# Kernel optimization log

Hardware: AMD Instinct MI355X
Metric: run time of the kernel (lower is better)

Reference implementation:

```python
import jax, jax.numpy as jnp
import numpy as np

B, L, D = 4096, 50, 128          # users, neighbors/user, embed_dim
N_U, N_I, N_R, N_T = 10000, 100000, 6, 1000
EPS = 1e-5                       # BatchNorm eps (eval mode, running stats)


def setup_inputs() -> dict:
    key = jax.random.key(0)
    ks = iter(jax.random.split(key, 80))
    nk = lambda: next(ks)

    def lin(din, dout):
        s = 1.0 / np.sqrt(din)
        w = jax.random.uniform(nk(), (din, dout), minval=-s, maxval=s, dtype=jnp.float32)
        b = jax.random.uniform(nk(), (dout,), minval=-s, maxval=s, dtype=jnp.float32)
        return w, b

    inp = {}
    # embedding tables (u2e/i2e/r2e/t2e)
    inp['u2e'] = 0.1 * jax.random.normal(nk(), (N_U, D), jnp.float32)
    inp['i2e'] = 0.1 * jax.random.normal(nk(), (N_I, D), jnp.float32)
    inp['r2e'] = 0.1 * jax.random.normal(nk(), (N_R, D), jnp.float32)
    inp['t2e'] = 0.1 * jax.random.normal(nk(), (N_T, D), jnp.float32)
    # neighbor transform MLP
    inp['ne_w'], inp['ne_b'] = lin(3 * D, D)
    inp['ne1_w'], inp['ne1_b'] = lin(D, D)
    # attention MLP (NewAttention: concat(neigh, user) -> D -> D -> 1, softmax over neighbors)
    inp['att1_w'], inp['att1_b'] = lin(2 * D, D)
    inp['att2_w'], inp['att2_b'] = lin(D, D)
    inp['att3_w'], inp['att3_b'] = lin(D, 1)
    # head
    inp['lin_w'], inp['lin_b'] = lin(2 * D, D)
    inp['w1_w'], inp['w1_b'] = lin(D, D // 4)
    inp['bn1_g'] = jnp.ones((D // 4,), jnp.float32)
    inp['bn1_b'] = jnp.zeros((D // 4,), jnp.float32)
    inp['bn1_m'] = 0.1 * jax.random.normal(nk(), (D // 4,), jnp.float32)
    inp['bn1_v'] = jax.random.uniform(nk(), (D // 4,), minval=0.5, maxval=1.5, dtype=jnp.float32)
    inp['w2_w'], inp['w2_b'] = lin(D // 4, D // 8)
    inp['bn2_g'] = jnp.ones((D // 8,), jnp.float32)
    inp['bn2_b'] = jnp.zeros((D // 8,), jnp.float32)
    inp['bn2_m'] = 0.1 * jax.random.normal(nk(), (D // 8,), jnp.float32)
    inp['bn2_v'] = jax.random.uniform(nk(), (D // 8,), minval=0.5, maxval=1.5, dtype=jnp.float32)
    inp['w3_w'], inp['w3_b'] = lin(D // 8, 1)
    # index inputs (padded-fixed neighbor lists)
    inp['user_idx'] = jax.random.randint(nk(), (B,), 0, N_U)
    inp['item_idx'] = jax.random.randint(nk(), (B, L), 0, N_I)
    inp['rat_idx'] = jax.random.randint(nk(), (B, L), 0, N_R)
    inp['time_idx'] = jax.random.randint(nk(), (B, L), 0, N_T)
    return inp


def reference(u2e, i2e, r2e, t2e, ne_w, ne_b, ne1_w, ne1_b,
              att1_w, att1_b, att2_w, att2_b, att3_w, att3_b,
              lin_w, lin_b, w1_w, w1_b, bn1_g, bn1_b, bn1_m, bn1_v,
              w2_w, w2_b, bn2_g, bn2_b, bn2_m, bn2_v, w3_w, w3_b,
              user_idx, item_idx, rat_idx, time_idx):
    u = u2e[user_idx]                                                   # [B, D]
    neigh = jnp.concatenate([i2e[item_idx], r2e[rat_idx], t2e[time_idx]], axis=-1)  # [B, L, 3D]
    x = jax.nn.relu(neigh @ ne_w + ne_b)                                # [B, L, D]
    x = jax.nn.relu(x @ ne1_w + ne1_b)                                  # [B, L, D]
    # attention over neighbors, conditioned on the user embedding
    a = jnp.concatenate([x, jnp.broadcast_to(u[:, None, :], x.shape)], axis=-1)  # [B, L, 2D]
    a = jax.nn.relu(a @ att1_w + att1_b)
    a = jax.nn.relu(a @ att2_w + att2_b)
    att = jax.nn.softmax((a @ att3_w + att3_b)[..., 0], axis=-1)        # [B, L]
    pooled = jnp.einsum('bl,bld->bd', att, x)                           # torch.mm(x.t(), att).t()
    comb = jax.nn.relu(jnp.concatenate([u, pooled], axis=-1) @ lin_w + lin_b)  # [B, D]
    h = comb @ w1_w + w1_b
    h = jax.nn.relu((h - bn1_m) * jax.lax.rsqrt(bn1_v + EPS) * bn1_g + bn1_b)
    h = h @ w2_w + w2_b
    h = jax.nn.relu((h - bn2_m) * jax.lax.rsqrt(bn2_v + EPS) * bn2_g + bn2_b)
    return (h @ w3_w + w3_b)[:, 0]                                      # [B]
```

## Files before the change

kernel.cpp:

```cpp
#include <hip/hip_runtime.h>
#include <hip/hip_bf16.h>

typedef __bf16 bf16x8 __attribute__((ext_vector_type(8)));
typedef float  f32x4  __attribute__((ext_vector_type(4)));

#define W_OFF 0
#define A_OFF 16384
#define X_OFF 29696
#define SMALL 43008
#define SMEM_TOTAL 47104
#define WCHUNK 16384
#define WHALF  8192

#define WS_WPREP 0
#define WS_PI    262144
#define WS_PT    (WS_PI + 25600000)
#define WS_PR    (WS_PT + 512000)
#define WS_PU    (WS_PR + 3072)
#define WS_PU2   (WS_PU + 5120000)

__global__ void prep_weights_kernel(const float* __restrict__ ne_w,
                                    const float* __restrict__ ne1_w,
                                    const float* __restrict__ att1_w,
                                    const float* __restrict__ att2_w,
                                    const float* __restrict__ lin_w,
                                    __hip_bfloat16* __restrict__ wout) {
  __shared__ float tile[64][65];
  const int bx = blockIdx.x;
  const int c = bx >> 2, kt = (bx >> 1) & 1, ntile = bx & 1;
  const float* src; int koff;
  if      (c < 3)  { src = ne_w;   koff = c * 128; }
  else if (c == 3) { src = ne1_w;  koff = 0; }
  else if (c == 4) { src = att1_w; koff = 0; }
  else if (c == 5) { src = att2_w; koff = 0; }
  else if (c == 6) { src = att1_w; koff = 128; }
  else             { src = lin_w;  koff = 0; }
  const int tx = threadIdx.x, ty = threadIdx.y;
#pragma unroll
  for (int r = 0; r < 16; ++r) {
    int k = kt * 64 + r * 4 + ty, n = ntile * 64 + tx;
    tile[r * 4 + ty][tx] = src[(koff + k) * 128 + n];
  }
  __syncthreads();
#pragma unroll
  for (int r = 0; r < 16; ++r) {
    int n = ntile * 64 + r * 4 + ty, k = kt * 64 + tx;
    int h = k >> 6, k64 = k & 63;
    int off = c * WCHUNK + h * WHALF + n * 64 + ((((k64 >> 3) ^ (n & 7))) << 3) + (k64 & 7);
    wout[off] = __float2bfloat16(tile[tx][r * 4 + ty]);
  }
}

__device__ __forceinline__ unsigned short bf_bits(float x) {
  return __builtin_bit_cast(unsigned short, __float2bfloat16(x));
}

__device__ __forceinline__ void mfma_half(const __hip_bfloat16* sIn,
                                          const __hip_bfloat16* sWh,
                                          f32x4 acc[4], int h, int m16, int nh, int lane) {
  const int mr = lane & 15;
  const int kq = lane >> 4;
  const int arow = (m16 * 16 + mr) * 128;
#pragma unroll
  for (int ks = 0; ks < 2; ++ks) {
    const int kb16 = h * 8 + ks * 4 + kq;
    bf16x8 a = *(const bf16x8*)(sIn + arow + ((kb16 ^ mr) << 3));
    const int swzb = (((ks * 4 + kq) ^ (mr & 7)) << 3);
#pragma unroll
    for (int nt = 0; nt < 4; ++nt) {
      const int n = nh * 64 + nt * 16 + mr;
      bf16x8 b = *(const bf16x8*)(sWh + n * 64 + swzb);
      acc[nt] = __builtin_amdgcn_mfma_f32_16x16x32_bf16(a, b, acc[nt], 0, 0, 0);
    }
  }
}

__device__ __forceinline__ void epilogue(f32x4 acc[4], const float* __restrict__ bias,
                                         const float* addvec, __hip_bfloat16* sOut,
                                         int m16, int nh, int lane) {
  const int mr = lane & 15;
  const int rb = m16 * 16 + ((lane >> 4) << 2);
#pragma unroll
  for (int nt = 0; nt < 4; ++nt) {
    const int col = nh * 64 + nt * 16 + mr;
    float bv = bias[col];
    if (addvec) bv += addvec[col];
    const int cblk = col >> 3, clo = col & 7;
#pragma unroll
    for (int r = 0; r < 4; ++r) {
      const int row = rb + r;
      if (row < 50) {
        float v = fmaxf(acc[nt][r] + bv, 0.0f);
        sOut[row * 128 + ((cblk ^ (row & 15)) << 3) + clo] = __float2bfloat16(v);
      }
    }
  }
}

__global__ __launch_bounds__(512) void pgemm_kernel(
    const float* __restrict__ i2e, const float* __restrict__ r2e,
    const float* __restrict__ t2e, const float* __restrict__ u2e,
    const float* __restrict__ ne_b, const __hip_bfloat16* __restrict__ wprep,
    __hip_bfloat16* __restrict__ Pi, float* __restrict__ Pt, float* __restrict__ Pr,
    float* __restrict__ Pu, float* __restrict__ Pu2) {
  __shared__ __align__(16) __hip_bfloat16 sW[WCHUNK];
  __shared__ __align__(16) __hip_bfloat16 sA[64 * 128];
  const int tid = threadIdx.x, lane = tid & 63, wid = tid >> 6;
  const int m16 = wid & 3, nh = wid >> 2;
  const int bx = blockIdx.x;
  const float* src; const __hip_bfloat16* W; float* dst = nullptr;
  const float* addb = nullptr; bool bf_out = false;
  long rows0; int nrows;
  if (bx < 1563)      { src = i2e; W = wprep + 0 * WCHUNK; bf_out = true; rows0 = (long)bx * 64;          nrows = 100000; }
  else if (bx < 1579) { src = t2e; W = wprep + 2 * WCHUNK; dst = Pt;  rows0 = (long)(bx - 1563) * 64; nrows = 1000; }
  else if (bx < 1580) { src = r2e; W = wprep + 1 * WCHUNK; dst = Pr;  rows0 = 0;                      nrows = 6; addb = ne_b; }
  else if (bx < 1737) { src = u2e; W = wprep + 6 * WCHUNK; dst = Pu;  rows0 = (long)(bx - 1580) * 64; nrows = 10000; }
  else                { src = u2e; W = wprep + 7 * WCHUNK; dst = Pu2; rows0 = (long)(bx - 1737) * 64; nrows = 10000; }

#pragma unroll
  for (int i = 0; i < 4; ++i) {
    int g = tid + i * 512;
    __builtin_amdgcn_global_load_lds(
        (__attribute__((address_space(1))) void*)(void*)(W + g * 8),
        (__attribute__((address_space(3))) void*)(void*)(sW + g * 8), 16, 0, 0);
  }
  const float4* s4 = (const float4*)src;
#pragma unroll
  for (int i = 0; i < 2; ++i) {
    int g = tid + i * 512;
    int row = g >> 4, kb = g & 15;
    float4 v0 = {0.f, 0.f, 0.f, 0.f}, v1 = {0.f, 0.f, 0.f, 0.f};
    if (rows0 + row < nrows) {
      long base = (rows0 + row) * 32 + kb * 2;
      v0 = s4[base]; v1 = s4[base + 1];
    }
    uint4 pk;
    pk.x = ((unsigned)bf_bits(v0.y) << 16) | bf_bits(v0.x);
    pk.y = ((unsigned)bf_bits(v0.w) << 16) | bf_bits(v0.z);
    pk.z = ((unsigned)bf_bits(v1.y) << 16) | bf_bits(v1.x);
    pk.w = ((unsigned)bf_bits(v1.w) << 16) | bf_bits(v1.z);
    *(uint4*)(sA + row * 128 + ((kb ^ (row & 15)) << 3)) = pk;
  }
  __syncthreads();

  f32x4 acc[4];
#pragma unroll
  for (int j = 0; j < 4; ++j) acc[j] = (f32x4){0.f, 0.f, 0.f, 0.f};
  mfma_half(sA, sW, acc, 0, m16, nh, lane);
  mfma_half(sA, sW + WHALF, acc, 1, m16, nh, lane);

  const int mr = lane & 15;
  const int rb = m16 * 16 + ((lane >> 4) << 2);
#pragma unroll
  for (int nt = 0; nt < 4; ++nt) {
    const int col = nh * 64 + nt * 16 + mr;
    const float bv = addb ? addb[col] : 0.f;
#pragma unroll
    for (int r = 0; r < 4; ++r) {
      const int row = rb + r;
      if (rows0 + row < nrows) {
        if (bf_out) Pi[(rows0 + row) * 128 + col] = __float2bfloat16(acc[nt][r]);
        else        dst[(rows0 + row) * 128 + col] = acc[nt][r] + bv;
      }
    }
  }
}

__global__ __launch_bounds__(512, 6) void graphdec_main(
    const __hip_bfloat16* __restrict__ Pi, const float* __restrict__ Pt,
    const float* __restrict__ Pr, const float* __restrict__ Pu,
    const float* __restrict__ Pu2,
    const float* __restrict__ ne1_b, const float* __restrict__ att1_b,
    const float* __restrict__ att2_b, const float* __restrict__ att3_w,
    const float* __restrict__ lin_w, const float* __restrict__ lin_b,
    const float* __restrict__ w1_w, const float* __restrict__ w1_b,
    const float* __restrict__ bn1_g, const float* __restrict__ bn1_b,
    const float* __restrict__ bn1_m, const float* __restrict__ bn1_v,
    const float* __restrict__ w2_w, const float* __restrict__ w2_b,
    const float* __restrict__ bn2_g, const float* __restrict__ bn2_b,
    const float* __restrict__ bn2_m, const float* __restrict__ bn2_v,
    const float* __restrict__ w3_w, const float* __restrict__ w3_b,
    const int* __restrict__ user_idx, const int* __restrict__ item_idx,
    const int* __restrict__ rat_idx, const int* __restrict__ time_idx,
    const __hip_bfloat16* __restrict__ wprep, float* __restrict__ out) {
  __shared__ __align__(16) unsigned char smem[SMEM_TOTAL];
  __hip_bfloat16* sW = (__hip_bfloat16*)(smem + W_OFF);
  __hip_bfloat16* sA = (__hip_bfloat16*)(smem + A_OFF);
  __hip_bfloat16* sX = (__hip_bfloat16*)(smem + X_OFF);
  int*   sIdx   = (int*)  (smem + SMALL);
  float* sUatt  = (float*)(smem + SMALL + 768);
  float* sUlin  = (float*)(smem + SMALL + 1280);
  float* sLP0   = (float*)(smem + SMALL + 1792);
  float* sLP1   = (float*)(smem + SMALL + 2048);
  float* sAtt   = (float*)(smem + SMALL + 2304);
  float* sPooled= (float*)(smem + SMALL + 2560);
  float* sComb  = (float*)(smem + SMALL + 3072);
  float* sH1    = (float*)(smem + SMALL + 3584);
  float* sPool4 = (float*)(smem + W_OFF);
  float* sCombP = (float*)(smem + W_OFF + 2048);

  const int tid  = threadIdx.x;
  const int lane = tid & 63;
  const int wid  = tid >> 6;
  const int m16  = wid & 3;
  const int nh   = wid >> 2;
  const int b    = blockIdx.x;

  float att3r[4];
#pragma unroll
  for (int nt = 0; nt < 4; ++nt) att3r[nt] = att3_w[nh * 64 + nt * 16 + (lane & 15)];

  if (tid < 192) {
    int c = tid >> 6, l = tid & 63;
    int v = 0;
    if (l < 50) {
      const int* p = (c == 0) ? item_idx : (c == 1) ? rat_idx : time_idx;
      v = p[b * 50 + l];
    }
    sIdx[tid] = v;
  }
  const int uid = user_idx[b];
  if (tid >= 256 && tid < 384)      sUatt[tid - 256] = Pu [(long)uid * 128 + (tid - 256)];
  else if (tid >= 384)              sUlin[tid - 384] = Pu2[(long)uid * 128 + (tid - 384)];
  __syncthreads();

  auto stage16 = [&](const __hip_bfloat16* __restrict__ src) {
#pragma unroll
    for (int i = 0; i < 2; ++i) {
      int g = tid + i * 512;
      __builtin_amdgcn_global_load_lds(
          (__attribute__((address_space(1))) void*)(void*)(src + g * 8),
          (__attribute__((address_space(3))) void*)(void*)(sW + g * 8), 16, 0, 0);
    }
  };

  f32x4 acc[4];
  const f32x4 zf = {0.f, 0.f, 0.f, 0.f};
  auto zacc = [&]() {
#pragma unroll
    for (int j = 0; j < 4; ++j) acc[j] = zf;
  };

  stage16(wprep + 3 * WCHUNK);
#pragma unroll
  for (int i = 0; i < 2; ++i) {
    int g = tid + i * 512;
    if (g < 832) {
      int row = g >> 4, kb = g & 15;
      uint4 pk = {0u, 0u, 0u, 0u};
      if (row < 50) {
        const bf16x8 pv = *(const bf16x8*)(Pi + (long)sIdx[row] * 128 + kb * 8);
        const float4* pr4 = (const float4*)(Pr + (long)sIdx[64 + row] * 128) + kb * 2;
        const float4* pt4 = (const float4*)(Pt + (long)sIdx[128 + row] * 128) + kb * 2;
        float4 r0 = pr4[0], r1 = pr4[1];
        float4 t0 = pt4[0], t1 = pt4[1];
        float s0 = fmaxf((float)pv[0] + r0.x + t0.x, 0.f);
        float s1 = fmaxf((float)pv[1] + r0.y + t0.y, 0.f);
        float s2 = fmaxf((float)pv[2] + r0.z + t0.z, 0.f);
        float s3 = fmaxf((float)pv[3] + r0.w + t0.w, 0.f);
        float s4 = fmaxf((float)pv[4] + r1.x + t1.x, 0.f);
        float s5 = fmaxf((float)pv[5] + r1.y + t1.y, 0.f);
        float s6 = fmaxf((float)pv[6] + r1.z + t1.z, 0.f);
        float s7 = fmaxf((float)pv[7] + r1.w + t1.w, 0.f);
        pk.x = ((unsigned)bf_bits(s1) << 16) | bf_bits(s0);
        pk.y = ((unsigned)bf_bits(s3) << 16) | bf_bits(s2);
        pk.z = ((unsigned)bf_bits(s5) << 16) | bf_bits(s4);
        pk.w = ((unsigned)bf_bits(s7) << 16) | bf_bits(s6);
      }
      *(uint4*)(sA + row * 128 + ((kb ^ (row & 15)) << 3)) = pk;
    }
  }
  __syncthreads();

  zacc();
  mfma_half(sA, sW, acc, 0, m16, nh, lane);
  __syncthreads();
  stage16(wprep + 3 * WCHUNK + WHALF);
  __syncthreads();
  mfma_half(sA, sW, acc, 1, m16, nh, lane);
  __syncthreads();
  stage16(wprep + 4 * WCHUNK);
  epilogue(acc, ne1_b, nullptr, sX, m16, nh, lane);
  __syncthreads();

  zacc();
  mfma_half(sX, sW, acc, 0, m16, nh, lane);
  __syncthreads();
  stage16(wprep + 4 * WCHUNK + WHALF);
  __syncthreads();
  mfma_half(sX, sW, acc, 1, m16, nh, lane);
  __syncthreads();
  stage16(wprep + 5 * WCHUNK);
  epilogue(acc, att1_b, sUatt, sA, m16, nh, lane);
  __syncthreads();

  zacc();
  mfma_half(sA, sW, acc, 0, m16, nh, lane);
  __syncthreads();
  stage16(wprep + 5 * WCHUNK + WHALF);
  __syncthreads();
  mfma_half(sA, sW, acc, 1, m16, nh, lane);
  {
    float lp[4] = {0.f, 0.f, 0.f, 0.f};
#pragma unroll
    for (int nt = 0; nt < 4; ++nt) {
      const int col = nh * 64 + nt * 16 + (lane & 15);
      const float b2 = att2_b[col];
#pragma unroll
      for (int r = 0; r < 4; ++r)
        lp[r] += fmaxf(acc[nt][r] + b2, 0.f) * att3r[nt];
    }
#pragma unroll
    for (int off = 1; off < 16; off <<= 1) {
#pragma unroll
      for (int r = 0; r < 4; ++r) lp[r] += __shfl_xor(lp[r], off);
    }
    if ((lane & 15) == 0) {
      const int rowb = m16 * 16 + ((lane >> 4) << 2);
      float* dst = nh ? sLP1 : sLP0;
#pragma unroll
      for (int r = 0; r < 4; ++r) dst[rowb + r] = lp[r];
    }
  }
  __syncthreads();

  if (wid == 0) {
    float v = (lane < 50) ? (sLP0[lane] + sLP1[lane]) : -3.4e38f;
    float m = v;
    for (int off = 32; off > 0; off >>= 1) m = fmaxf(m, __shfl_xor(m, off));
    float e = (lane < 50) ? __expf(v - m) : 0.f;
    float s = e;
    for (int off = 32; off > 0; off >>= 1) s += __shfl_xor(s, off);
    sAtt[lane] = e / s;
  }
  __syncthreads();

  {
    int q = tid >> 7, d = tid & 127;
    const int cblk = d >> 3, clo = d & 7;
    float s = 0.f;
    for (int l = q; l < 50; l += 4)
      s += sAtt[l] * (float)sX[l * 128 + ((cblk ^ (l & 15)) << 3) + clo];
    sPool4[q * 128 + d] = s;
  }
  __syncthreads();
  if (tid < 128)
    sPooled[tid] = sPool4[tid] + sPool4[128 + tid] + sPool4[256 + tid] + sPool4[384 + tid];
  __syncthreads();

  {
    int q = tid >> 7, d = tid & 127;
    float s = 0.f;
    for (int j = q * 32; j < q * 32 + 32; ++j) s += sPooled[j] * lin_w[(128 + j) * 128 + d];
    sCombP[q * 128 + d] = s;
  }
  __syncthreads();
  if (tid < 128)
    sComb[tid] = fmaxf(sCombP[tid] + sCombP[128 + tid] + sCombP[256 + tid] + sCombP[384 + tid]
                       + sUlin[tid] + lin_b[tid], 0.f);
  __syncthreads();

  if (wid == 0) {
    if (lane < 32) {
      float s = w1_b[lane];
      for (int k = 0; k < 128; ++k) s += sComb[k] * w1_w[k * 32 + lane];
      s = (s - bn1_m[lane]) * rsqrtf(bn1_v[lane] + 1e-5f) * bn1_g[lane] + bn1_b[lane];
      sH1[lane] = fmaxf(s, 0.f);
    }
    if (lane < 16) {
      float s = w2_b[lane];
      for (int k = 0; k < 32; ++k) s += sH1[k] * w2_w[k * 16 + lane];
      s = (s - bn2_m[lane]) * rsqrtf(bn2_v[lane] + 1e-5f) * bn2_g[lane] + bn2_b[lane];
      float p = fmaxf(s, 0.f) * w3_w[lane];
      p += __shfl_xor(p, 1); p += __shfl_xor(p, 2);
      p += __shfl_xor(p, 4); p += __shfl_xor(p, 8);
      if (lane == 0) out[b] = p + w3_b[0];
    }
  }
}

extern "C" void kernel_launch(void* const* d_in, const int* in_sizes, int n_in,
                              void* d_out, int out_size, void* d_ws, size_t ws_size,
                              hipStream_t stream) {
  const float* u2e    = (const float*)d_in[0];
  const float* i2e    = (const float*)d_in[1];
  const float* r2e    = (const float*)d_in[2];
  const float* t2e    = (const float*)d_in[3];
  const float* ne_w   = (const float*)d_in[4];
  const float* ne_b   = (const float*)d_in[5];
  const float* ne1_w  = (const float*)d_in[6];
  const float* ne1_b  = (const float*)d_in[7];
  const float* att1_w = (const float*)d_in[8];
  const float* att1_b = (const float*)d_in[9];
  const float* att2_w = (const float*)d_in[10];
  const float* att2_b = (const float*)d_in[11];
  const float* att3_w = (const float*)d_in[12];
  const float* att3_b = (const float*)d_in[13];
  const float* lin_w  = (const float*)d_in[14];
  const float* lin_b  = (const float*)d_in[15];
  const float* w1_w   = (const float*)d_in[16];
  const float* w1_b   = (const float*)d_in[17];
  const float* bn1_g  = (const float*)d_in[18];
  const float* bn1_b  = (const float*)d_in[19];
  const float* bn1_m  = (const float*)d_in[20];
  const float* bn1_v  = (const float*)d_in[21];
  const float* w2_w   = (const float*)d_in[22];
  const float* w2_b   = (const float*)d_in[23];
  const float* bn2_g  = (const float*)d_in[24];
  const float* bn2_b  = (const float*)d_in[25];
  const float* bn2_m  = (const float*)d_in[26];
  const float* bn2_v  = (const float*)d_in[27];
  const float* w3_w   = (const float*)d_in[28];
  const float* w3_b   = (const float*)d_in[29];
  const int* user_idx = (const int*)d_in[30];
  const int* item_idx = (const int*)d_in[31];
  const int* rat_idx  = (const int*)d_in[32];
  const int* time_idx = (const int*)d_in[33];
  (void)att3_b;

  char* ws = (char*)d_ws;
  __hip_bfloat16* wprep = (__hip_bfloat16*)(ws + WS_WPREP);
  __hip_bfloat16* Pi = (__hip_bfloat16*)(ws + WS_PI);
  float* Pt  = (float*)(ws + WS_PT);
  float* Pr  = (float*)(ws + WS_PR);
  float* Pu  = (float*)(ws + WS_PU);
  float* Pu2 = (float*)(ws + WS_PU2);
  float* out = (float*)d_out;

  prep_weights_kernel<<<32, dim3(64, 4), 0, stream>>>(ne_w, ne1_w, att1_w, att2_w,
                                                      lin_w, wprep);
  pgemm_kernel<<<1894, 512, 0, stream>>>(i2e, r2e, t2e, u2e, ne_b, wprep,
                                         Pi, Pt, Pr, Pu, Pu2);
  graphdec_main<<<4096, 512, 0, stream>>>(
      Pi, Pt, Pr, Pu, Pu2, ne1_b, att1_b, att2_b, att3_w,
      lin_w, lin_b, w1_w, w1_b, bn1_g, bn1_b, bn1_m, bn1_v, w2_w, w2_b,
      bn2_g, bn2_b, bn2_m, bn2_v, w3_w, w3_b,
      user_idx, item_idx, rat_idx, time_idx, wprep, out);
}
```

Measured before the change: 242.3 us.

## Process two users per block to share staged weight tiles

Each graphdec_main block now handles two users instead of one. Four waves serve each user, and each wave computes all 128 output columns (8 MFMA tiles) rather than splitting N across waves. Every weight chunk staged into LDS is therefore reused across two users, which halves the weight staging traffic and the number of blocks. The cost is more LDS per block (about 77KB), twice the accumulator registers, and a lowered occupancy hint (4 instead of 6), which may reduce latency hiding for the gathers.

```diff
diff --git a/kernel.cpp b/kernel.cpp
--- a/kernel.cpp
+++ b/kernel.cpp
@@ -6,9 +6,9 @@
 
 #define W_OFF 0
 #define A_OFF 16384
-#define X_OFF 29696
-#define SMALL 43008
-#define SMEM_TOTAL 47104
+#define X_OFF 43008
+#define SMALL 69632
+#define SMEM_TOTAL 77824
 #define WCHUNK 16384
 #define WHALF  8192
 
@@ -55,6 +55,48 @@
   return __builtin_bit_cast(unsigned short, __float2bfloat16(x));
 }
 
+__device__ __forceinline__ void mfma_half8(const __hip_bfloat16* sIn,
+                                           const __hip_bfloat16* sWh,
+                                           f32x4 acc[8], int h, int m16, int lane) {
+  const int mr = lane & 15;
+  const int kq = lane >> 4;
+  const int arow = (m16 * 16 + mr) * 128;
+#pragma unroll
+  for (int ks = 0; ks < 2; ++ks) {
+    const int kb16 = h * 8 + ks * 4 + kq;
+    bf16x8 a = *(const bf16x8*)(sIn + arow + ((kb16 ^ mr) << 3));
+    const int swzb = (((ks * 4 + kq) ^ (mr & 7)) << 3);
+#pragma unroll
+    for (int nt = 0; nt < 8; ++nt) {
+      const int n = nt * 16 + mr;
+      bf16x8 b = *(const bf16x8*)(sWh + n * 64 + swzb);
+      acc[nt] = __builtin_amdgcn_mfma_f32_16x16x32_bf16(a, b, acc[nt], 0, 0, 0);
+    }
+  }
+}
+
+__device__ __forceinline__ void epilogue8(f32x4 acc[8], const float* __restrict__ bias,
+                                          const float* addvec, __hip_bfloat16* sOut,
+                                          int m16, int lane) {
+  const int mr = lane & 15;
+  const int rb = m16 * 16 + ((lane >> 4) << 2);
+#pragma unroll
+  for (int nt = 0; nt < 8; ++nt) {
+    const int col = nt * 16 + mr;
+    float bv = bias[col];
+    if (addvec) bv += addvec[col];
+    const int cblk = col >> 3, clo = col & 7;
+#pragma unroll
+    for (int r = 0; r < 4; ++r) {
+      const int row = rb + r;
+      if (row < 50) {
+        float v = fmaxf(acc[nt][r] + bv, 0.0f);
+        sOut[row * 128 + ((cblk ^ (row & 15)) << 3) + clo] = __float2bfloat16(v);
+      }
+    }
+  }
+}
+
 __device__ __forceinline__ void mfma_half(const __hip_bfloat16* sIn,
                                           const __hip_bfloat16* sWh,
                                           f32x4 acc[4], int h, int m16, int nh, int lane) {
@@ -71,28 +113,6 @@
       const int n = nh * 64 + nt * 16 + mr;
       bf16x8 b = *(const bf16x8*)(sWh + n * 64 + swzb);
       acc[nt] = __builtin_amdgcn_mfma_f32_16x16x32_bf16(a, b, acc[nt], 0, 0, 0);
-    }
-  }
-}
-
-__device__ __forceinline__ void epilogue(f32x4 acc[4], const float* __restrict__ bias,
-                                         const float* addvec, __hip_bfloat16* sOut,
-                                         int m16, int nh, int lane) {
-  const int mr = lane & 15;
-  const int rb = m16 * 16 + ((lane >> 4) << 2);
-#pragma unroll
-  for (int nt = 0; nt < 4; ++nt) {
-    const int col = nh * 64 + nt * 16 + mr;
-    float bv = bias[col];
-    if (addvec) bv += addvec[col];
-    const int cblk = col >> 3, clo = col & 7;
-#pragma unroll
-    for (int r = 0; r < 4; ++r) {
-      const int row = rb + r;
-      if (row < 50) {
-        float v = fmaxf(acc[nt][r] + bv, 0.0f);
-        sOut[row * 128 + ((cblk ^ (row & 15)) << 3) + clo] = __float2bfloat16(v);
-      }
     }
   }
 }
@@ -166,7 +186,7 @@
   }
 }
 
-__global__ __launch_bounds__(512, 6) void graphdec_main(
+__global__ __launch_bounds__(512, 4) void graphdec_main(
     const __hip_bfloat16* __restrict__ Pi, const float* __restrict__ Pt,
     const float* __restrict__ Pr, const float* __restrict__ Pu,
     const float* __restrict__ Pu2,
@@ -185,43 +205,54 @@
     const __hip_bfloat16* __restrict__ wprep, float* __restrict__ out) {
   __shared__ __align__(16) unsigned char smem[SMEM_TOTAL];
   __hip_bfloat16* sW = (__hip_bfloat16*)(smem + W_OFF);
-  __hip_bfloat16* sA = (__hip_bfloat16*)(smem + A_OFF);
-  __hip_bfloat16* sX = (__hip_bfloat16*)(smem + X_OFF);
-  int*   sIdx   = (int*)  (smem + SMALL);
-  float* sUatt  = (float*)(smem + SMALL + 768);
-  float* sUlin  = (float*)(smem + SMALL + 1280);
-  float* sLP0   = (float*)(smem + SMALL + 1792);
-  float* sLP1   = (float*)(smem + SMALL + 2048);
-  float* sAtt   = (float*)(smem + SMALL + 2304);
-  float* sPooled= (float*)(smem + SMALL + 2560);
-  float* sComb  = (float*)(smem + SMALL + 3072);
-  float* sH1    = (float*)(smem + SMALL + 3584);
-  float* sPool4 = (float*)(smem + W_OFF);
-  float* sCombP = (float*)(smem + W_OFF + 2048);
 
   const int tid  = threadIdx.x;
   const int lane = tid & 63;
   const int wid  = tid >> 6;
+  const int uw   = wid >> 2;
   const int m16  = wid & 3;
-  const int nh   = wid >> 2;
-  const int b    = blockIdx.x;
-
-  float att3r[4];
-#pragma unroll
-  for (int nt = 0; nt < 4; ++nt) att3r[nt] = att3_w[nh * 64 + nt * 16 + (lane & 15)];
-
-  if (tid < 192) {
-    int c = tid >> 6, l = tid & 63;
+  const int ut   = tid >> 8;
+  const int t256 = tid & 255;
+  const long b   = blockIdx.x;
+
+  __hip_bfloat16* sAw = (__hip_bfloat16*)(smem + A_OFF + uw * 13312);
+  __hip_bfloat16* sXw = (__hip_bfloat16*)(smem + X_OFF + uw * 13312);
+  __hip_bfloat16* sAt = (__hip_bfloat16*)(smem + A_OFF + ut * 13312);
+  __hip_bfloat16* sXt = (__hip_bfloat16*)(smem + X_OFF + ut * 13312);
+  unsigned char* sSmW = smem + SMALL + uw * 4096;
+  unsigned char* sSmT = smem + SMALL + ut * 4096;
+  int*   sIdxT   = (int*)  (sSmT);
+  float* sUattW  = (float*)(sSmW + 768);
+  float* sUlinT  = (float*)(sSmT + 1280);
+  float* sLPW    = (float*)(sSmW + 1792);
+  float* sLPU    = (float*)(sSmW + 1792);
+  float* sAttT   = (float*)(sSmT + 2048);
+  float* sPooledT= (float*)(sSmT + 2304);
+  float* sCombT  = (float*)(sSmT + 2816);
+  float* sCombW  = (float*)(sSmW + 2816);
+  float* sH1W    = (float*)(sSmW + 3328);
+  float* sPool2T = (float*)(smem + W_OFF + ut * 8192);
+  float* sCombPT = (float*)(smem + W_OFF + ut * 8192 + 4096);
+
+  float att3r[8];
+#pragma unroll
+  for (int nt = 0; nt < 8; ++nt) att3r[nt] = att3_w[nt * 16 + (lane & 15)];
+
+  if (t256 < 192) {
+    int c = t256 >> 6, l = t256 & 63;
     int v = 0;
     if (l < 50) {
       const int* p = (c == 0) ? item_idx : (c == 1) ? rat_idx : time_idx;
-      v = p[b * 50 + l];
-    }
-    sIdx[tid] = v;
-  }
-  const int uid = user_idx[b];
-  if (tid >= 256 && tid < 384)      sUatt[tid - 256] = Pu [(long)uid * 128 + (tid - 256)];
-  else if (tid >= 384)              sUlin[tid - 384] = Pu2[(long)uid * 128 + (tid - 384)];
+      v = p[(b * 2 + ut) * 50 + l];
+    }
+    sIdxT[t256] = v;
+  }
+  {
+    const int uid = user_idx[b * 2 + ut];
+    float* sUattT = (float*)(sSmT + 768);
+    if (t256 < 128) sUattT[t256]       = Pu [(long)uid * 128 + t256];
+    else            sUlinT[t256 - 128] = Pu2[(long)uid * 128 + (t256 - 128)];
+  }
   __syncthreads();
 
   auto stage16 = [&](const __hip_bfloat16* __restrict__ src) {
@@ -234,24 +265,24 @@
     }
   };
 
-  f32x4 acc[4];
+  f32x4 acc[8];
   const f32x4 zf = {0.f, 0.f, 0.f, 0.f};
   auto zacc = [&]() {
 #pragma unroll
-    for (int j = 0; j < 4; ++j) acc[j] = zf;
+    for (int j = 0; j < 8; ++j) acc[j] = zf;
   };
 
   stage16(wprep + 3 * WCHUNK);
 #pragma unroll
-  for (int i = 0; i < 2; ++i) {
-    int g = tid + i * 512;
+  for (int i = 0; i < 4; ++i) {
+    int g = t256 + i * 256;
     if (g < 832) {
       int row = g >> 4, kb = g & 15;
       uint4 pk = {0u, 0u, 0u, 0u};
       if (row < 50) {
-        const bf16x8 pv = *(const bf16x8*)(Pi + (long)sIdx[row] * 128 + kb * 8);
-        const float4* pr4 = (const float4*)(Pr + (long)sIdx[64 + row] * 128) + kb * 2;
-        const float4* pt4 = (const float4*)(Pt + (long)sIdx[128 + row] * 128) + kb * 2;
+        const bf16x8 pv = *(const bf16x8*)(Pi + (long)sIdxT[row] * 128 + kb * 8);
+        const float4* pr4 = (const float4*)(Pr + (long)sIdxT[64 + row] * 128) + kb * 2;
+        const float4* pt4 = (const float4*)(Pt + (long)sIdxT[128 + row] * 128) + kb * 2;
         float4 r0 = pr4[0], r1 = pr4[1];
         float4 t0 = pt4[0], t1 = pt4[1];
         float s0 = fmaxf((float)pv[0] + r0.x + t0.x, 0.f);
@@ -267,44 +298,44 @@
         pk.z = ((unsigned)bf_bits(s5) << 16) | bf_bits(s4);
         pk.w = ((unsigned)bf_bits(s7) << 16) | bf_bits(s6);
       }
-      *(uint4*)(sA + row * 128 + ((kb ^ (row & 15)) << 3)) = pk;
+      *(uint4*)(sAt + row * 128 + ((kb ^ (row & 15)) << 3)) = pk;
     }
   }
   __syncthreads();
 
   zacc();
-  mfma_half(sA, sW, acc, 0, m16, nh, lane);
+  mfma_half8(sAw, sW, acc, 0, m16, lane);
   __syncthreads();
   stage16(wprep + 3 * WCHUNK + WHALF);
   __syncthreads();
-  mfma_half(sA, sW, acc, 1, m16, nh, lane);
+  mfma_half8(sAw, sW, acc, 1, m16, lane);
   __syncthreads();
   stage16(wprep + 4 * WCHUNK);
-  epilogue(acc, ne1_b, nullptr, sX, m16, nh, lane);
+  epilogue8(acc, ne1_b, nullptr, sXw, m16, lane);
   __syncthreads();
 
   zacc();
-  mfma_half(sX, sW, acc, 0, m16, nh, lane);
+  mfma_half8(sXw, sW, acc, 0, m16, lane);
   __syncthreads();
   stage16(wprep + 4 * WCHUNK + WHALF);
   __syncthreads();
-  mfma_half(sX, sW, acc, 1, m16, nh, lane);
+  mfma_half8(sXw, sW, acc, 1, m16, lane);
   __syncthreads();
   stage16(wprep + 5 * WCHUNK);
-  epilogue(acc, att1_b, sUatt, sA, m16, nh, lane);
+  epilogue8(acc, att1_b, sUattW, sAw, m16, lane);
   __syncthreads();
 
   zacc();
-  mfma_half(sA, sW, acc, 0, m16, nh, lane);
+  mfma_half8(sAw, sW, acc, 0, m16, lane);
   __syncthreads();
   stage16(wprep + 5 * WCHUNK + WHALF);
   __syncthreads();
-  mfma_half(sA, sW, acc, 1, m16, nh, lane);
+  mfma_half8(sAw, sW, acc, 1, m16, lane);
   {
     float lp[4] = {0.f, 0.f, 0.f, 0.f};
 #pragma unroll
-    for (int nt = 0; nt < 4; ++nt) {
-      const int col = nh * 64 + nt * 16 + (lane & 15);
+    for (int nt = 0; nt < 8; ++nt) {
+      const int col = nt * 16 + (lane & 15);
       const float b2 = att2_b[col];
 #pragma unroll
       for (int r = 0; r < 4; ++r)
@@ -317,64 +348,64 @@
     }
     if ((lane & 15) == 0) {
       const int rowb = m16 * 16 + ((lane >> 4) << 2);
-      float* dst = nh ? sLP1 : sLP0;
-#pragma unroll
-      for (int r = 0; r < 4; ++r) dst[rowb + r] = lp[r];
-    }
-  }
-  __syncthreads();
-
-  if (wid == 0) {
-    float v = (lane < 50) ? (sLP0[lane] + sLP1[lane]) : -3.4e38f;
+#pragma unroll
+      for (int r = 0; r < 4; ++r) sLPW[rowb + r] = lp[r];
+    }
+  }
+  __syncthreads();
+
+  if (m16 == 0) {
+    float v = (lane < 50) ? sLPU[lane] : -3.4e38f;
     float m = v;
     for (int off = 32; off > 0; off >>= 1) m = fmaxf(m, __shfl_xor(m, off));
     float e = (lane < 50) ? __expf(v - m) : 0.f;
     float s = e;
     for (int off = 32; off > 0; off >>= 1) s += __shfl_xor(s, off);
-    sAtt[lane] = e / s;
+    float* sAttW = (float*)(sSmW + 2048);
+    sAttW[lane] = e / s;
   }
   __syncthreads();
 
   {
-    int q = tid >> 7, d = tid & 127;
+    int q = t256 >> 7, d = t256 & 127;
     const int cblk = d >> 3, clo = d & 7;
     float s = 0.f;
-    for (int l = q; l < 50; l += 4)
-      s += sAtt[l] * (float)sX[l * 128 + ((cblk ^ (l & 15)) << 3) + clo];
-    sPool4[q * 128 + d] = s;
-  }
-  __syncthreads();
-  if (tid < 128)
-    sPooled[tid] = sPool4[tid] + sPool4[128 + tid] + sPool4[256 + tid] + sPool4[384 + tid];
+    for (int l = q; l < 50; l += 2)
+      s += sAttT[l] * (float)sXt[l * 128 + ((cblk ^ (l & 15)) << 3) + clo];
+    sPool2T[q * 128 + d] = s;
+  }
+  __syncthreads();
+  if (t256 < 128)
+    sPooledT[t256] = sPool2T[t256] + sPool2T[128 + t256];
   __syncthreads();
 
   {
-    int q = tid >> 7, d = tid & 127;
+    int q = t256 >> 7, d = t256 & 127;
     float s = 0.f;
-    for (int j = q * 32; j < q * 32 + 32; ++j) s += sPooled[j] * lin_w[(128 + j) * 128 + d];
-    sCombP[q * 128 + d] = s;
-  }
-  __syncthreads();
-  if (tid < 128)
-    sComb[tid] = fmaxf(sCombP[tid] + sCombP[128 + tid] + sCombP[256 + tid] + sCombP[384 + tid]
-                       + sUlin[tid] + lin_b[tid], 0.f);
-  __syncthreads();
-
-  if (wid == 0) {
+    for (int j = q * 64; j < q * 64 + 64; ++j) s += sPooledT[j] * lin_w[(128 + j) * 128 + d];
+    sCombPT[q * 128 + d] = s;
+  }
+  __syncthreads();
+  if (t256 < 128)
+    sCombT[t256] = fmaxf(sCombPT[t256] + sCombPT[128 + t256]
+                         + sUlinT[t256] + lin_b[t256], 0.f);
+  __syncthreads();
+
+  if (m16 == 0) {
     if (lane < 32) {
       float s = w1_b[lane];
-      for (int k = 0; k < 128; ++k) s += sComb[k] * w1_w[k * 32 + lane];
+      for (int k = 0; k < 128; ++k) s += sCombW[k] * w1_w[k * 32 + lane];
       s = (s - bn1_m[lane]) * rsqrtf(bn1_v[lane] + 1e-5f) * bn1_g[lane] + bn1_b[lane];
-      sH1[lane] = fmaxf(s, 0.f);
+      sH1W[lane] = fmaxf(s, 0.f);
     }
     if (lane < 16) {
       float s = w2_b[lane];
-      for (int k = 0; k < 32; ++k) s += sH1[k] * w2_w[k * 16 + lane];
+      for (int k = 0; k < 32; ++k) s += sH1W[k] * w2_w[k * 16 + lane];
       s = (s - bn2_m[lane]) * rsqrtf(bn2_v[lane] + 1e-5f) * bn2_g[lane] + bn2_b[lane];
       float p = fmaxf(s, 0.f) * w3_w[lane];
       p += __shfl_xor(p, 1); p += __shfl_xor(p, 2);
       p += __shfl_xor(p, 4); p += __shfl_xor(p, 8);
-      if (lane == 0) out[b] = p + w3_b[0];
+      if (lane == 0) out[b * 2 + uw] = p + w3_b[0];
     }
   }
 }
@@ -431,7 +462,7 @@
                                                       lin_w, wprep);
   pgemm_kernel<<<1894, 512, 0, stream>>>(i2e, r2e, t2e, u2e, ne_b, wprep,
                                          Pi, Pt, Pr, Pu, Pu2);
-  graphdec_main<<<4096, 512, 0, stream>>>(
+  graphdec_main<<<2048, 512, 0, stream>>>(
       Pi, Pt, Pr, Pu, Pu2, ne1_b, att1_b, att2_b, att3_w,
       lin_w, lin_b, w1_w, w1_b, bn1_g, bn1_b, bn1_m, bn1_v, w2_w, w2_b,
       bn2_g, bn2_b, bn2_m, bn2_v, w3_w, w3_b,
```

New measurement: 249.3 us. +2.9%, slower.

## Keep ne1 activations in registers, share one LDS activation buffer, raise occupancy

Applied to the files above, without the earlier changes.

The separate sX LDS buffer is removed, so the ne1 layer output both overwrites the single activation buffer and stays in fp32 registers (facc). The attention-weighted pooling is now computed from those registers with cross-lane shuffles instead of re-reading bf16 values from LDS. The smaller LDS footprint, together with launch bounds raised from 6 to 8, is meant to allow more resident blocks per CU. The risk is that the 16 extra live accumulators under a tighter register budget cause spills.

```diff
diff --git a/kernel.cpp b/kernel.cpp
--- a/kernel.cpp
+++ b/kernel.cpp
@@ -4,11 +4,10 @@
 typedef __bf16 bf16x8 __attribute__((ext_vector_type(8)));
 typedef float  f32x4  __attribute__((ext_vector_type(4)));
 
-#define W_OFF 0
-#define A_OFF 16384
-#define X_OFF 29696
-#define SMALL 43008
-#define SMEM_TOTAL 47104
+#define W_OFF   0
+#define ACT_OFF 16384
+#define SMALL   29696
+#define SMEM_TOTAL 33792
 #define WCHUNK 16384
 #define WHALF  8192
 
@@ -166,7 +165,7 @@
   }
 }
 
-__global__ __launch_bounds__(512, 6) void graphdec_main(
+__global__ __launch_bounds__(512, 8) void graphdec_main(
     const __hip_bfloat16* __restrict__ Pi, const float* __restrict__ Pt,
     const float* __restrict__ Pr, const float* __restrict__ Pu,
     const float* __restrict__ Pu2,
@@ -184,9 +183,8 @@
     const int* __restrict__ rat_idx, const int* __restrict__ time_idx,
     const __hip_bfloat16* __restrict__ wprep, float* __restrict__ out) {
   __shared__ __align__(16) unsigned char smem[SMEM_TOTAL];
-  __hip_bfloat16* sW = (__hip_bfloat16*)(smem + W_OFF);
-  __hip_bfloat16* sA = (__hip_bfloat16*)(smem + A_OFF);
-  __hip_bfloat16* sX = (__hip_bfloat16*)(smem + X_OFF);
+  __hip_bfloat16* sW   = (__hip_bfloat16*)(smem + W_OFF);
+  __hip_bfloat16* sAct = (__hip_bfloat16*)(smem + ACT_OFF);
   int*   sIdx   = (int*)  (smem + SMALL);
   float* sUatt  = (float*)(smem + SMALL + 768);
   float* sUlin  = (float*)(smem + SMALL + 1280);
@@ -232,13 +230,6 @@
           (__attribute__((address_space(1))) void*)(void*)(src + g * 8),
           (__attribute__((address_space(3))) void*)(void*)(sW + g * 8), 16, 0, 0);
     }
-  };
-
-  f32x4 acc[4];
-  const f32x4 zf = {0.f, 0.f, 0.f, 0.f};
-  auto zacc = [&]() {
-#pragma unroll
-    for (int j = 0; j < 4; ++j) acc[j] = zf;
   };
 
   stage16(wprep + 3 * WCHUNK);
@@ -267,39 +258,64 @@
         pk.z = ((unsigned)bf_bits(s5) << 16) | bf_bits(s4);
         pk.w = ((unsigned)bf_bits(s7) << 16) | bf_bits(s6);
       }
-      *(uint4*)(sA + row * 128 + ((kb ^ (row & 15)) << 3)) = pk;
-    }
-  }
-  __syncthreads();
-
-  zacc();
-  mfma_half(sA, sW, acc, 0, m16, nh, lane);
+      *(uint4*)(sAct + row * 128 + ((kb ^ (row & 15)) << 3)) = pk;
+    }
+  }
+  __syncthreads();
+
+  const f32x4 zf = {0.f, 0.f, 0.f, 0.f};
+
+  f32x4 facc[4];
+#pragma unroll
+  for (int j = 0; j < 4; ++j) facc[j] = zf;
+  mfma_half(sAct, sW, facc, 0, m16, nh, lane);
   __syncthreads();
   stage16(wprep + 3 * WCHUNK + WHALF);
   __syncthreads();
-  mfma_half(sA, sW, acc, 1, m16, nh, lane);
+  mfma_half(sAct, sW, facc, 1, m16, nh, lane);
   __syncthreads();
   stage16(wprep + 4 * WCHUNK);
-  epilogue(acc, ne1_b, nullptr, sX, m16, nh, lane);
-  __syncthreads();
-
-  zacc();
-  mfma_half(sX, sW, acc, 0, m16, nh, lane);
+  {
+    const int mr = lane & 15;
+    const int rb = m16 * 16 + ((lane >> 4) << 2);
+#pragma unroll
+    for (int nt = 0; nt < 4; ++nt) {
+      const int col = nh * 64 + nt * 16 + mr;
+      const float bv = ne1_b[col];
+      const int cblk = col >> 3, clo = col & 7;
+#pragma unroll
+      for (int r = 0; r < 4; ++r) {
+        const int row = rb + r;
+        float v = fmaxf(facc[nt][r] + bv, 0.0f);
+        v = (row < 50) ? v : 0.0f;
+        facc[nt][r] = v;
+        if (row < 50)
+          sAct[row * 128 + ((cblk ^ (row & 15)) << 3) + clo] = __float2bfloat16(v);
+      }
+    }
+  }
+  __syncthreads();
+
+  f32x4 acc[4];
+#pragma unroll
+  for (int j = 0; j < 4; ++j) acc[j] = zf;
+  mfma_half(sAct, sW, acc, 0, m16, nh, lane);
   __syncthreads();
   stage16(wprep + 4 * WCHUNK + WHALF);
   __syncthreads();
-  mfma_half(sX, sW, acc, 1, m16, nh, lane);
+  mfma_half(sAct, sW, acc, 1, m16, nh, lane);
   __syncthreads();
   stage16(wprep + 5 * WCHUNK);
-  epilogue(acc, att1_b, sUatt, sA, m16, nh, lane);
-  __syncthreads();
-
-  zacc();
-  mfma_half(sA, sW, acc, 0, m16, nh, lane);
+  epilogue(acc, att1_b, sUatt, sAct, m16, nh, lane);
+  __syncthreads();
+
+#pragma unroll
+  for (int j = 0; j < 4; ++j) acc[j] = zf;
+  mfma_half(sAct, sW, acc, 0, m16, nh, lane);
   __syncthreads();
   stage16(wprep + 5 * WCHUNK + WHALF);
   __syncthreads();
-  mfma_half(sA, sW, acc, 1, m16, nh, lane);
+  mfma_half(sAct, sW, acc, 1, m16, nh, lane);
   {
     float lp[4] = {0.f, 0.f, 0.f, 0.f};
 #pragma unroll
@@ -336,12 +352,16 @@
   __syncthreads();
 
   {
-    int q = tid >> 7, d = tid & 127;
-    const int cblk = d >> 3, clo = d & 7;
-    float s = 0.f;
-    for (int l = q; l < 50; l += 4)
-      s += sAtt[l] * (float)sX[l * 128 + ((cblk ^ (l & 15)) << 3) + clo];
-    sPool4[q * 128 + d] = s;
+    const int mr = lane & 15;
+    const int rb = m16 * 16 + ((lane >> 4) << 2);
+    float a0 = sAtt[rb], a1 = sAtt[rb + 1], a2 = sAtt[rb + 2], a3 = sAtt[rb + 3];
+#pragma unroll
+    for (int nt = 0; nt < 4; ++nt) {
+      float s = a0 * facc[nt][0] + a1 * facc[nt][1] + a2 * facc[nt][2] + a3 * facc[nt][3];
+      s += __shfl_xor(s, 16);
+      s += __shfl_xor(s, 32);
+      if (lane < 16) sPool4[m16 * 128 + nh * 64 + nt * 16 + mr] = s;
+    }
   }
   __syncthreads();
   if (tid < 128)
```

After: 297.2 us. +22.6%, slower.

## Read GEMM weights directly from global memory instead of staging through LDS

Applied to the files above, without the earlier changes.

Removes the LDS weight buffer and its half-chunk staging loop with global_load_lds. The three per-neighbor GEMMs now read swizzled bf16 weights straight from global (L2/L1-cached) memory, which also drops several block-wide barriers. Shared memory per block shrinks from about 47 KB to 30 KB, and the launch-bounds occupancy hint changes from 6 to 4. The trade is that every wave now issues its own global loads for B fragments, so latency that was amortized across the block is exposed per wave.

```diff
diff --git a/kernel.cpp b/kernel.cpp
--- a/kernel.cpp
+++ b/kernel.cpp
@@ -4,11 +4,10 @@
 typedef __bf16 bf16x8 __attribute__((ext_vector_type(8)));
 typedef float  f32x4  __attribute__((ext_vector_type(4)));
 
-#define W_OFF 0
-#define A_OFF 16384
-#define X_OFF 29696
-#define SMALL 43008
-#define SMEM_TOTAL 47104
+#define A_OFF   0
+#define X_OFF   13312
+#define SMALL   26624
+#define SMEM_TOTAL 30720
 #define WCHUNK 16384
 #define WHALF  8192
 
@@ -53,6 +52,29 @@
 
 __device__ __forceinline__ unsigned short bf_bits(float x) {
   return __builtin_bit_cast(unsigned short, __float2bfloat16(x));
+}
+
+__device__ __forceinline__ void mfma_gemm(const __hip_bfloat16* sIn,
+                                          const __hip_bfloat16* __restrict__ W,
+                                          f32x4 acc[4], int m16, int nh, int lane) {
+  const int mr = lane & 15;
+  const int kq = lane >> 4;
+  const int arow = (m16 * 16 + mr) * 128;
+#pragma unroll
+  for (int h = 0; h < 2; ++h) {
+#pragma unroll
+    for (int ks = 0; ks < 2; ++ks) {
+      const int kb16 = h * 8 + ks * 4 + kq;
+      bf16x8 a = *(const bf16x8*)(sIn + arow + ((kb16 ^ mr) << 3));
+      const int swzb = (((ks * 4 + kq) ^ (mr & 7)) << 3);
+#pragma unroll
+      for (int nt = 0; nt < 4; ++nt) {
+        const int n = nh * 64 + nt * 16 + mr;
+        bf16x8 b = *(const bf16x8*)(W + h * WHALF + n * 64 + swzb);
+        acc[nt] = __builtin_amdgcn_mfma_f32_16x16x32_bf16(a, b, acc[nt], 0, 0, 0);
+      }
+    }
+  }
 }
 
 __device__ __forceinline__ void mfma_half(const __hip_bfloat16* sIn,
@@ -166,7 +188,7 @@
   }
 }
 
-__global__ __launch_bounds__(512, 6) void graphdec_main(
+__global__ __launch_bounds__(512, 4) void graphdec_main(
     const __hip_bfloat16* __restrict__ Pi, const float* __restrict__ Pt,
     const float* __restrict__ Pr, const float* __restrict__ Pu,
     const float* __restrict__ Pu2,
@@ -184,7 +206,6 @@
     const int* __restrict__ rat_idx, const int* __restrict__ time_idx,
     const __hip_bfloat16* __restrict__ wprep, float* __restrict__ out) {
   __shared__ __align__(16) unsigned char smem[SMEM_TOTAL];
-  __hip_bfloat16* sW = (__hip_bfloat16*)(smem + W_OFF);
   __hip_bfloat16* sA = (__hip_bfloat16*)(smem + A_OFF);
   __hip_bfloat16* sX = (__hip_bfloat16*)(smem + X_OFF);
   int*   sIdx   = (int*)  (smem + SMALL);
@@ -196,8 +217,8 @@
   float* sPooled= (float*)(smem + SMALL + 2560);
   float* sComb  = (float*)(smem + SMALL + 3072);
   float* sH1    = (float*)(smem + SMALL + 3584);
-  float* sPool4 = (float*)(smem + W_OFF);
-  float* sCombP = (float*)(smem + W_OFF + 2048);
+  float* sPool4 = (float*)(smem + A_OFF);
+  float* sCombP = (float*)(smem + A_OFF + 2048);
 
   const int tid  = threadIdx.x;
   const int lane = tid & 63;
@@ -224,24 +245,6 @@
   else if (tid >= 384)              sUlin[tid - 384] = Pu2[(long)uid * 128 + (tid - 384)];
   __syncthreads();
 
-  auto stage16 = [&](const __hip_bfloat16* __restrict__ src) {
-#pragma unroll
-    for (int i = 0; i < 2; ++i) {
-      int g = tid + i * 512;
-      __builtin_amdgcn_global_load_lds(
-          (__attribute__((address_space(1))) void*)(void*)(src + g * 8),
-          (__attribute__((address_space(3))) void*)(void*)(sW + g * 8), 16, 0, 0);
-    }
-  };
-
-  f32x4 acc[4];
-  const f32x4 zf = {0.f, 0.f, 0.f, 0.f};
-  auto zacc = [&]() {
-#pragma unroll
-    for (int j = 0; j < 4; ++j) acc[j] = zf;
-  };
-
-  stage16(wprep + 3 * WCHUNK);
 #pragma unroll
   for (int i = 0; i < 2; ++i) {
     int g = tid + i * 512;
@@ -272,34 +275,24 @@
   }
   __syncthreads();
 
-  zacc();
-  mfma_half(sA, sW, acc, 0, m16, nh, lane);
-  __syncthreads();
-  stage16(wprep + 3 * WCHUNK + WHALF);
-  __syncthreads();
-  mfma_half(sA, sW, acc, 1, m16, nh, lane);
-  __syncthreads();
-  stage16(wprep + 4 * WCHUNK);
+  f32x4 acc[4];
+  const f32x4 zf = {0.f, 0.f, 0.f, 0.f};
+
+#pragma unroll
+  for (int j = 0; j < 4; ++j) acc[j] = zf;
+  mfma_gemm(sA, wprep + 3 * WCHUNK, acc, m16, nh, lane);
   epilogue(acc, ne1_b, nullptr, sX, m16, nh, lane);
   __syncthreads();
 
-  zacc();
-  mfma_half(sX, sW, acc, 0, m16, nh, lane);
-  __syncthreads();
-  stage16(wprep + 4 * WCHUNK + WHALF);
-  __syncthreads();
-  mfma_half(sX, sW, acc, 1, m16, nh, lane);
-  __syncthreads();
-  stage16(wprep + 5 * WCHUNK);
+#pragma unroll
+  for (int j = 0; j < 4; ++j) acc[j] = zf;
+  mfma_gemm(sX, wprep + 4 * WCHUNK, acc, m16, nh, lane);
   epilogue(acc, att1_b, sUatt, sA, m16, nh, lane);
   __syncthreads();
 
-  zacc();
-  mfma_half(sA, sW, acc, 0, m16, nh, lane);
-  __syncthreads();
-  stage16(wprep + 5 * WCHUNK + WHALF);
-  __syncthreads();
-  mfma_half(sA, sW, acc, 1, m16, nh, lane);
+#pragma unroll
+  for (int j = 0; j < 4; ++j) acc[j] = zf;
+  mfma_gemm(sA, wprep + 5 * WCHUNK, acc, m16, nh, lane);
   {
     float lp[4] = {0.f, 0.f, 0.f, 0.f};
 #pragma unroll
```

New measurement: 292.0 us. +20.5%, slower.
